# Kernel tuning notes

Hardware: AMD Instinct MI355X
Metric: run time of the kernel (lower is better)

The kernel has to match this reference:

```python
import jax, jax.numpy as jnp
import numpy as np

B, S, D = 32, 1024, 512
LN_EPS = 1e-5


def setup_inputs() -> dict:
    key = jax.random.key(0)
    ks = jax.random.split(key, 12)
    scale = 1.0 / np.sqrt(D)
    return {
        "seq1": jax.random.normal(ks[0], (B, S, D), jnp.float32),
        "seq2": jax.random.normal(ks[1], (B, S, D), jnp.float32),
        "mask1": jax.random.randint(ks[2], (B, S), 0, 2) == 1,
        "mask2": jax.random.randint(ks[3], (B, S), 0, 2) == 1,
        "Wq": jax.random.uniform(ks[4], (D, D), jnp.float32, -scale, scale),
        "bq": jax.random.uniform(ks[5], (D,), jnp.float32, -scale, scale),
        "Wk": jax.random.uniform(ks[6], (D, D), jnp.float32, -scale, scale),
        "bk": jax.random.uniform(ks[7], (D,), jnp.float32, -scale, scale),
        "Wv": jax.random.uniform(ks[8], (D, D), jnp.float32, -scale, scale),
        "bv": jax.random.uniform(ks[9], (D,), jnp.float32, -scale, scale),
        "gamma": jnp.ones((D,), jnp.float32),
        "beta": jnp.zeros((D,), jnp.float32),
    }


def _layernorm(x, gamma, beta):
    mu = jnp.mean(x, axis=-1, keepdims=True)
    var = jnp.mean(jnp.square(x - mu), axis=-1, keepdims=True)
    return (x - mu) * jax.lax.rsqrt(var + LN_EPS) * gamma + beta


def reference(seq1, seq2, mask1, mask2, Wq, bq, Wk, bk, Wv, bv, gamma, beta):
    # relu-projected Q/K/V (shared weights across both sequences)
    q1 = jax.nn.relu(seq1 @ Wq + bq)
    k1 = jax.nn.relu(seq1 @ Wk + bk)
    v1 = jax.nn.relu(seq1 @ Wv + bv)
    q2 = jax.nn.relu(seq2 @ Wq + bq)
    k2 = jax.nn.relu(seq2 @ Wk + bk)
    v2 = jax.nn.relu(seq2 @ Wv + bv)

    # bilinear cross scores: tanh(k1 q2^T) summed over seq2 -> [B,S1]
    a1 = jnp.sum(jnp.tanh(jnp.einsum('bsd,btd->bst', k1, q2)), axis=2)
    a2 = jnp.sum(jnp.tanh(jnp.einsum('btd,bsd->bts', k2, q1)), axis=2)

    a1 = jnp.where(mask1, -jnp.inf, a1)
    a2 = jnp.where(mask2, -jnp.inf, a2)
    a1 = jax.nn.softmax(a1, axis=-1)  # [B,S1]
    a2 = jax.nn.softmax(a2, axis=-1)  # [B,S2]
    # dropout p=0.2 is identity at inference

    vector1 = jnp.einsum('bs,bsd->bd', a1, v1)
    vector2 = jnp.einsum('bs,bsd->bd', a2, v2)

    out1 = _layernorm(jnp.mean(seq1, axis=1) + vector1, gamma, beta)
    out2 = _layernorm(jnp.mean(seq2, axis=1) + vector2, gamma, beta)
    return (out1, out2)
```

## Files before the change

### kernel.cpp

```cpp
#include <hip/hip_runtime.h>


typedef __bf16 bf16x8_t __attribute__((ext_vector_type(8)));
typedef float f32x4_t __attribute__((ext_vector_type(4)));

__device__ __forceinline__ unsigned short f2bf(float f) {
    union { float f; unsigned int u; } c; c.f = f;
    unsigned int u = c.u;
    unsigned int r = (u + 0x7FFFu + ((u >> 16) & 1u)) >> 16;
    return (unsigned short)r;
}
__device__ __forceinline__ float bf2f(unsigned short h) {
    union { unsigned int u; float f; } c; c.u = ((unsigned int)h) << 16;
    return c.f;
}
__device__ __forceinline__ void gl2lds16(const void* g, void* l) {
    __builtin_amdgcn_global_load_lds(
        (const __attribute__((address_space(1))) void*)g,
        (__attribute__((address_space(3))) void*)l, 16, 0, 0);
}
__device__ __forceinline__ float fast_tanh(float x) {
    float e = __expf(2.f * x);
    return 1.f - 2.f * __builtin_amdgcn_rcpf(e + 1.f);
}

__device__ __forceinline__ void stage256(
    const unsigned short* __restrict__ src,
    int k0, unsigned short* dstbase, int wv, int lane)
{
    #pragma unroll
    for (int l = 0; l < 4; ++l) {
        int idx = l * 512 + wv * 64 + lane;
        int row = idx >> 3;
        int kc = (idx & 7) * 8;
        kc ^= ((row >> 2) & 1) << 4;
        gl2lds16(&src[(size_t)row * 512 + k0 + kc],
                 &dstbase[l * 4096 + wv * 512]);
    }
}

template<bool DRAIN>
__device__ __forceinline__ void phase_mfma(
    const unsigned short* A_, const unsigned short* B_,
    f32x4_t acc[8][4], int mh, int nh, int wr, int wc, int qq, int ln)
{
    bf16x8_t af[4][2], bfr[2][2];
    #pragma unroll
    for (int m = 0; m < 4; ++m) {
        int row = wr * 128 + (mh * 4 + m) * 16 + ln;
        #pragma unroll
        for (int ks = 0; ks < 2; ++ks) {
            int e = (row * 64 + ks * 32 + qq * 8) ^ (((row >> 2) & 1) << 4);
            af[m][ks] = *reinterpret_cast<const bf16x8_t*>(&A_[e]);
        }
    }
    #pragma unroll
    for (int n = 0; n < 2; ++n) {
        int row = wc * 64 + (nh * 2 + n) * 16 + ln;
        #pragma unroll
        for (int ks = 0; ks < 2; ++ks) {
            int e = (row * 64 + ks * 32 + qq * 8) ^ (((row >> 2) & 1) << 4);
            bfr[n][ks] = *reinterpret_cast<const bf16x8_t*>(&B_[e]);
        }
    }
    __builtin_amdgcn_s_barrier();
    __builtin_amdgcn_s_setprio(1);
    #pragma unroll
    for (int m = 0; m < 4; ++m)
        #pragma unroll
        for (int n = 0; n < 2; ++n)
            #pragma unroll
            for (int ks = 0; ks < 2; ++ks)
                acc[mh * 4 + m][nh * 2 + n] =
                    __builtin_amdgcn_mfma_f32_16x16x32_bf16(
                        af[m][ks], bfr[n][ks], acc[mh * 4 + m][nh * 2 + n],
                        0, 0, 0);
    __builtin_amdgcn_s_setprio(0);
    if (DRAIN) __syncthreads();
    else       __builtin_amdgcn_s_barrier();
}

#define GEMM256_MAINLOOP(Asrc, Bsrc)                                          \
    stage256(Asrc, 0, &lds[0][0][0], wv, lane);                               \
    stage256(Bsrc, 0, &lds[0][1][0], wv, lane);                               \
    __syncthreads();                                                          \
    _Pragma("unroll")                                                         \
    for (int i = 0; i < 4; ++i) {                                             \
        int kO = (2 * i + 1) * 64;                                            \
        int kE = (2 * i + 2) * 64;                                            \
            \
        stage256(Asrc, kO, &lds[1][0][0], wv, lane);                          \
        phase_mfma<false>(&lds[0][0][0], &lds[0][1][0], acc, 0, 0, wr, wc, qq, ln); \
        stage256(Bsrc, kO, &lds[1][1][0], wv, lane);                          \
        phase_mfma<false>(&lds[0][0][0], &lds[0][1][0], acc, 0, 1, wr, wc, qq, ln); \
        phase_mfma<false>(&lds[0][0][0], &lds[0][1][0], acc, 1, 0, wr, wc, qq, ln); \
        phase_mfma<true >(&lds[0][0][0], &lds[0][1][0], acc, 1, 1, wr, wc, qq, ln); \
            \
        if (i < 3) stage256(Asrc, kE, &lds[0][0][0], wv, lane);               \
        phase_mfma<false>(&lds[1][0][0], &lds[1][1][0], acc, 0, 0, wr, wc, qq, ln); \
        if (i < 3) stage256(Bsrc, kE, &lds[0][1][0], wv, lane);               \
        phase_mfma<false>(&lds[1][0][0], &lds[1][1][0], acc, 0, 1, wr, wc, qq, ln); \
        phase_mfma<false>(&lds[1][0][0], &lds[1][1][0], acc, 1, 0, wr, wc, qq, ln); \
        phase_mfma<true >(&lds[1][0][0], &lds[1][1][0], acc, 1, 1, wr, wc, qq, ln); \
    }

__global__ __launch_bounds__(256) void x2bf_kernel(
    const float* __restrict__ src, unsigned short* __restrict__ dst,
    float* __restrict__ accv)
{
    int chunk = blockIdx.x;
    int b = blockIdx.y;
    int tid = threadIdx.x, lane = tid & 63, wv = tid >> 6;
    __shared__ float red[4][512];
    float sum[8] = {};
    size_t base = ((size_t)b * 1024 + (size_t)chunk * 128) * 512;
    #pragma unroll 4
    for (int i = 0; i < 32; ++i) {
        int r = i * 4 + wv;
        size_t ro = base + (size_t)r * 512;
        float4 a = *reinterpret_cast<const float4*>(&src[ro + lane * 4]);
        float4 c = *reinterpret_cast<const float4*>(&src[ro + 256 + lane * 4]);
        ushort4 ha; ha.x = f2bf(a.x); ha.y = f2bf(a.y); ha.z = f2bf(a.z); ha.w = f2bf(a.w);
        ushort4 hc; hc.x = f2bf(c.x); hc.y = f2bf(c.y); hc.z = f2bf(c.z); hc.w = f2bf(c.w);
        *reinterpret_cast<ushort4*>(&dst[ro + lane * 4]) = ha;
        *reinterpret_cast<ushort4*>(&dst[ro + 256 + lane * 4]) = hc;
        sum[0] += a.x; sum[1] += a.y; sum[2] += a.z; sum[3] += a.w;
        sum[4] += c.x; sum[5] += c.y; sum[6] += c.z; sum[7] += c.w;
    }
    #pragma unroll
    for (int t = 0; t < 4; ++t) {
        red[wv][lane * 4 + t] = sum[t];
        red[wv][256 + lane * 4 + t] = sum[4 + t];
    }
    __syncthreads();
    #pragma unroll
    for (int j = 0; j < 2; ++j) {
        int col = tid + j * 256;
        float s = red[0][col] + red[1][col] + red[2][col] + red[3][col];
        atomicAdd(&accv[(size_t)b * 512 + col], s * (1.f / 1024.f));
    }
}

__global__ __launch_bounds__(256) void wconv_kernel(
    const float* __restrict__ Wq, const float* __restrict__ Wk,
    const float* __restrict__ Wv, unsigned short* __restrict__ Wt)
{
    const float* W = (blockIdx.z == 0) ? Wq : (blockIdx.z == 1) ? Wk : Wv;
    unsigned short* o = Wt + (size_t)blockIdx.z * 512 * 512;
    __shared__ unsigned short t[64][65];
    int k0 = blockIdx.x * 64, n0 = blockIdx.y * 64;
    #pragma unroll
    for (int i = 0; i < 16; ++i) {
        int idx = i * 256 + threadIdx.x;
        int r = idx >> 6, c = idx & 63;
        t[r][c] = f2bf(W[(size_t)(k0 + r) * 512 + n0 + c]);
    }
    __syncthreads();
    #pragma unroll
    for (int i = 0; i < 16; ++i) {
        int idx = i * 256 + threadIdx.x;
        int r = idx >> 6, c = idx & 63;
        o[(size_t)(n0 + r) * 512 + k0 + c] = t[c][r];
    }
}

__global__ __launch_bounds__(512) void biascat_kernel(
    const float* __restrict__ bq, const float* __restrict__ bk,
    const float* __restrict__ bv, float* __restrict__ bc)
{
    int n = threadIdx.x;
    bc[n] = bq[n]; bc[512 + n] = bk[n]; bc[1024 + n] = bv[n];
}

__global__ __launch_bounds__(512, 2) void qkv_gemm(
    const unsigned short* __restrict__ Xb1, const unsigned short* __restrict__ Xb2,
    const unsigned short* __restrict__ Wt, const float* __restrict__ bias_cat,
    unsigned short* __restrict__ qkv)
{
    __shared__ alignas(16) unsigned short lds[2][2][16384];

    unsigned int fid = blockIdx.x;
    unsigned int swz = (fid & 7u) * 192u + (fid >> 3);
    int nt = swz % 6u;
    int mg = swz / 6u;
    int z = mg >> 7;
    int mrow0 = (mg & 127) * 256;
    int n0 = nt * 256;

    const unsigned short* Asrc = (z ? Xb2 : Xb1) + (size_t)mrow0 * 512;
    const unsigned short* Bsrc = Wt + (size_t)n0 * 512;

    int tid = threadIdx.x, lane = tid & 63, wv = tid >> 6;
    int wr = wv >> 2, wc = wv & 3;
    int qq = lane >> 4, ln = lane & 15;

    f32x4_t acc[8][4] = {};

    GEMM256_MAINLOOP(Asrc, Bsrc)

    unsigned short* Ct = &lds[0][0][0];
    #pragma unroll
    for (int ni = 0; ni < 4; ++ni) {
        int col = wc * 64 + ni * 16 + ln;
        float bb = bias_cat[n0 + col];
        #pragma unroll
        for (int mi = 0; mi < 8; ++mi) {
            int row = wr * 128 + mi * 16 + qq * 4;
            #pragma unroll
            for (int r = 0; r < 4; ++r)
                Ct[(row + r) * 256 + col] = f2bf(fmaxf(acc[mi][ni][r] + bb, 0.f));
        }
    }
    __syncthreads();
    int w = nt >> 1, col0 = (nt & 1) * 256;
    unsigned short* outb = qkv + (size_t)(z * 3 + w) * 32768 * 512
                               + (size_t)mrow0 * 512 + col0;
    #pragma unroll
    for (int it = 0; it < 16; ++it) {
        int row = it * 16 + (tid >> 5);
        int ch = tid & 31;
        *reinterpret_cast<uint4*>(&outb[(size_t)row * 512 + ch * 8]) =
            *reinterpret_cast<const uint4*>(&Ct[row * 256 + ch * 8]);
    }
}

__global__ __launch_bounds__(512, 2) void score_kernel(
    const unsigned short* __restrict__ qkv, float* __restrict__ a_out)
{
    __shared__ alignas(16) unsigned short lds[2][2][16384];

    unsigned int fid = blockIdx.x;
    unsigned int swz = (fid & 7u) * 128u + (fid >> 3);
    int tt = swz & 3, st = (swz >> 2) & 3;
    int z = swz >> 4;
    int which = z >> 5, b = z & 31;

    const unsigned short* Asrc =
        qkv + ((size_t)(which ? 4 : 1) * 32768 + (size_t)b * 1024 + st * 256) * 512;
    const unsigned short* Bsrc =
        qkv + ((size_t)(which ? 0 : 3) * 32768 + (size_t)b * 1024 + tt * 256) * 512;

    int tid = threadIdx.x, lane = tid & 63, wv = tid >> 6;
    int wr = wv >> 2, wc = wv & 3;
    int qq = lane >> 4, ln = lane & 15;

    f32x4_t acc[8][4] = {};

    GEMM256_MAINLOOP(Asrc, Bsrc)

    float* arow = a_out + (size_t)z * 1024 + st * 256 + wr * 128;
    #pragma unroll
    for (int mi = 0; mi < 8; ++mi) {
        #pragma unroll
        for (int r = 0; r < 4; ++r) {
            float s = 0.f;
            #pragma unroll
            for (int ni = 0; ni < 4; ++ni) s += fast_tanh(acc[mi][ni][r]);
            #pragma unroll
            for (int off = 1; off <= 8; off <<= 1) s += __shfl_xor(s, off, 64);
            if (ln == 0)
                atomicAdd(&arow[mi * 16 + qq * 4 + r], s);
        }
    }
}

__global__ __launch_bounds__(256) void softmax_kernel(
    const float* __restrict__ a_in, const int* __restrict__ mask1,
    const int* __restrict__ mask2, float* __restrict__ w_out)
{
    int z = blockIdx.x, which = z >> 5, b = z & 31;
    const int* mask = (which ? mask2 : mask1) + (size_t)b * 1024;
    const float* a = a_in + (size_t)z * 1024;
    float* w = w_out + (size_t)z * 1024;
    int tid = threadIdx.x, lane = tid & 63, wv = tid >> 6;

    float vals[4];
    #pragma unroll
    for (int j = 0; j < 4; ++j) {
        int s = tid + j * 256;
        vals[j] = mask[s] ? -__builtin_inff() : a[s];
    }
    float m = fmaxf(fmaxf(vals[0], vals[1]), fmaxf(vals[2], vals[3]));
    #pragma unroll
    for (int off = 32; off; off >>= 1) m = fmaxf(m, __shfl_xor(m, off, 64));
    __shared__ float redm[4], redsum[4];
    if (lane == 0) redm[wv] = m;
    __syncthreads();
    m = fmaxf(fmaxf(redm[0], redm[1]), fmaxf(redm[2], redm[3]));

    float e[4], sum = 0.f;
    #pragma unroll
    for (int j = 0; j < 4; ++j) { e[j] = __expf(vals[j] - m); sum += e[j]; }
    #pragma unroll
    for (int off = 32; off; off >>= 1) sum += __shfl_xor(sum, off, 64);
    if (lane == 0) redsum[wv] = sum;
    __syncthreads();
    sum = redsum[0] + redsum[1] + redsum[2] + redsum[3];
    float inv = 1.f / sum;
    #pragma unroll
    for (int j = 0; j < 4; ++j) w[tid + j * 256] = e[j] * inv;
}

__global__ __launch_bounds__(128) void wsum_kernel(
    const unsigned short* __restrict__ qkv, const float* __restrict__ w_in,
    float* __restrict__ acc)
{
    int chunk = blockIdx.x;
    int z = blockIdx.y, which = z >> 5, b = z & 31;
    const unsigned short* V =
        qkv + ((size_t)(which ? 5 : 2) * 32768 + (size_t)b * 1024) * 512;
    const float* w = w_in + (size_t)z * 1024;
    int d0 = threadIdx.x * 4;
    float a0 = 0.f, a1 = 0.f, a2 = 0.f, a3 = 0.f;
    int s0 = chunk * 128;
    #pragma unroll 4
    for (int s = s0; s < s0 + 128; ++s) {
        ushort4 v = *reinterpret_cast<const ushort4*>(&V[(size_t)s * 512 + d0]);
        float ws = w[s];
        a0 += ws * bf2f(v.x); a1 += ws * bf2f(v.y);
        a2 += ws * bf2f(v.z); a3 += ws * bf2f(v.w);
    }
    atomicAdd(&acc[(size_t)z * 512 + d0 + 0], a0);
    atomicAdd(&acc[(size_t)z * 512 + d0 + 1], a1);
    atomicAdd(&acc[(size_t)z * 512 + d0 + 2], a2);
    atomicAdd(&acc[(size_t)z * 512 + d0 + 3], a3);
}

__global__ __launch_bounds__(512) void ln_kernel(
    const float* __restrict__ acc, const float* __restrict__ gamma,
    const float* __restrict__ beta, float* __restrict__ out)
{
    int z = blockIdx.x, d = threadIdx.x;
    int lane = d & 63, wv = d >> 6;
    float x = acc[(size_t)z * 512 + d];
    float s = x;
    #pragma unroll
    for (int off = 32; off; off >>= 1) s += __shfl_xor(s, off, 64);
    __shared__ float red[8], red2[8];
    if (lane == 0) red[wv] = s;
    __syncthreads();
    float mu = 0.f;
    #pragma unroll
    for (int i = 0; i < 8; ++i) mu += red[i];
    mu *= (1.f / 512.f);
    float c = x - mu;
    float s2 = c * c;
    #pragma unroll
    for (int off = 32; off; off >>= 1) s2 += __shfl_xor(s2, off, 64);
    if (lane == 0) red2[wv] = s2;
    __syncthreads();
    float var = 0.f;
    #pragma unroll
    for (int i = 0; i < 8; ++i) var += red2[i];
    var *= (1.f / 512.f);
    out[(size_t)z * 512 + d] = c * __frsqrt_rn(var + 1e-5f) * gamma[d] + beta[d];
}

extern "C" void kernel_launch(void* const* d_in, const int* in_sizes, int n_in,
                              void* d_out, int out_size, void* d_ws, size_t ws_size,
                              hipStream_t stream) {
    const float* seq1 = (const float*)d_in[0];
    const float* seq2 = (const float*)d_in[1];
    const int* mask1 = (const int*)d_in[2];
    const int* mask2 = (const int*)d_in[3];
    const float* Wq = (const float*)d_in[4];
    const float* bq = (const float*)d_in[5];
    const float* Wk = (const float*)d_in[6];
    const float* bk = (const float*)d_in[7];
    const float* Wv = (const float*)d_in[8];
    const float* bv = (const float*)d_in[9];
    const float* gamma = (const float*)d_in[10];
    const float* beta = (const float*)d_in[11];
    float* out = (float*)d_out;

    char* ws = (char*)d_ws;
    float* a_sc = (float*)(ws);
    float* wsm = (float*)(ws + (256u << 10));
    float* accv = (float*)(ws + (512u << 10));
    float* bias_cat = (float*)(ws + (768u << 10));
    unsigned short* Wt = (unsigned short*)(ws + (1u << 20));
    unsigned short* Xb2 = (unsigned short*)(ws + (4ull << 20));
    unsigned short* qkv = (unsigned short*)(ws + (40ull << 20));
    unsigned short* Xb1 = (unsigned short*)d_in[1];

    hipMemsetAsync(ws, 0, 640u << 10, stream);

    wconv_kernel<<<dim3(8, 8, 3), 256, 0, stream>>>(Wq, Wk, Wv, Wt);
    biascat_kernel<<<1, 512, 0, stream>>>(bq, bk, bv, bias_cat);
    x2bf_kernel<<<dim3(8, 32), 256, 0, stream>>>(seq2, Xb2, accv + 32 * 512);
    x2bf_kernel<<<dim3(8, 32), 256, 0, stream>>>(seq1, Xb1, accv);
    qkv_gemm<<<dim3(1536), 512, 0, stream>>>(Xb1, Xb2, Wt, bias_cat, qkv);
    score_kernel<<<dim3(1024), 512, 0, stream>>>(qkv, a_sc);
    softmax_kernel<<<64, 256, 0, stream>>>(a_sc, mask1, mask2, wsm);
    wsum_kernel<<<dim3(8, 64), 128, 0, stream>>>(qkv, wsm, accv);
    ln_kernel<<<64, 512, 0, stream>>>(accv, gamma, beta, out);
}
```

Baseline: 490.3 us.

## Reuse A/B LDS fragments across MFMA quadrants and widen LDS XOR swizzle

Changes the LDS swizzle from a single-bit XOR on the 16-element chunk to a full 3-bit XOR of the 8-element slot index with the row, to reduce bank conflicts on fragment reads. It also restructures each K-step so A and B fragments are loaded once and reused across quadrants (a0 with b0/b1, a1 with b1/b0), instead of reloading both for every quadrant. The cost is more fragment registers live at once, which may raise register pressure and reduce occupancy.

Result: faster. 436.7 us (-10.9%).

```diff
diff --git a/kernel.cpp b/kernel.cpp
--- a/kernel.cpp
+++ b/kernel.cpp
@@ -32,38 +32,44 @@
     for (int l = 0; l < 4; ++l) {
         int idx = l * 512 + wv * 64 + lane;
         int row = idx >> 3;
-        int kc = (idx & 7) * 8;
-        kc ^= ((row >> 2) & 1) << 4;
-        gl2lds16(&src[(size_t)row * 512 + k0 + kc],
+        int slot = (idx & 7) ^ (row & 7);
+        gl2lds16(&src[(size_t)row * 512 + k0 + slot * 8],
                  &dstbase[l * 4096 + wv * 512]);
     }
 }
 
-template<bool DRAIN>
-__device__ __forceinline__ void phase_mfma(
-    const unsigned short* A_, const unsigned short* B_,
-    f32x4_t acc[8][4], int mh, int nh, int wr, int wc, int qq, int ln)
-{
-    bf16x8_t af[4][2], bfr[2][2];
+__device__ __forceinline__ void read_afrag(
+    const unsigned short* buf, int rbase, int qq, int ln, bf16x8_t af[4][2])
+{
     #pragma unroll
     for (int m = 0; m < 4; ++m) {
-        int row = wr * 128 + (mh * 4 + m) * 16 + ln;
+        int row = rbase + m * 16 + ln;
         #pragma unroll
         for (int ks = 0; ks < 2; ++ks) {
-            int e = (row * 64 + ks * 32 + qq * 8) ^ (((row >> 2) & 1) << 4);
-            af[m][ks] = *reinterpret_cast<const bf16x8_t*>(&A_[e]);
+            int slot = (ks * 4 + qq) ^ (ln & 7);
+            af[m][ks] = *reinterpret_cast<const bf16x8_t*>(
+                &buf[row * 64 + slot * 8]);
         }
     }
+}
+__device__ __forceinline__ void read_bfrag(
+    const unsigned short* buf, int rbase, int qq, int ln, bf16x8_t bfr[2][2])
+{
     #pragma unroll
     for (int n = 0; n < 2; ++n) {
-        int row = wc * 64 + (nh * 2 + n) * 16 + ln;
+        int row = rbase + n * 16 + ln;
         #pragma unroll
         for (int ks = 0; ks < 2; ++ks) {
-            int e = (row * 64 + ks * 32 + qq * 8) ^ (((row >> 2) & 1) << 4);
-            bfr[n][ks] = *reinterpret_cast<const bf16x8_t*>(&B_[e]);
+            int slot = (ks * 4 + qq) ^ (ln & 7);
+            bfr[n][ks] = *reinterpret_cast<const bf16x8_t*>(
+                &buf[row * 64 + slot * 8]);
         }
     }
-    __builtin_amdgcn_s_barrier();
+}
+__device__ __forceinline__ void mfma_quad(
+    const bf16x8_t a[4][2], const bf16x8_t b[2][2],
+    f32x4_t acc[8][4], int mh, int nh)
+{
     __builtin_amdgcn_s_setprio(1);
     #pragma unroll
     for (int m = 0; m < 4; ++m)
@@ -73,12 +79,28 @@
             for (int ks = 0; ks < 2; ++ks)
                 acc[mh * 4 + m][nh * 2 + n] =
                     __builtin_amdgcn_mfma_f32_16x16x32_bf16(
-                        af[m][ks], bfr[n][ks], acc[mh * 4 + m][nh * 2 + n],
-                        0, 0, 0);
+                        a[m][ks], b[n][ks], acc[mh * 4 + m][nh * 2 + n], 0, 0, 0);
     __builtin_amdgcn_s_setprio(0);
-    if (DRAIN) __syncthreads();
-    else       __builtin_amdgcn_s_barrier();
-}
+}
+
+#define GEMM256_HALF(CUR, NXT, SA, SB)                                        \
+    read_afrag(&lds[CUR][0][0], wr * 128, qq, ln, a0);                        \
+    read_bfrag(&lds[CUR][1][0], wc * 64, qq, ln, b0);                         \
+    SA;                                                                       \
+    __builtin_amdgcn_s_barrier();                                             \
+    mfma_quad(a0, b0, acc, 0, 0);                                             \
+    __builtin_amdgcn_s_barrier();                                             \
+    read_bfrag(&lds[CUR][1][0], wc * 64 + 32, qq, ln, b1);                    \
+    SB;                                                                       \
+    __builtin_amdgcn_s_barrier();                                             \
+    mfma_quad(a0, b1, acc, 0, 1);                                             \
+    __builtin_amdgcn_s_barrier();                                             \
+    read_afrag(&lds[CUR][0][0], wr * 128 + 64, qq, ln, a1);                   \
+    __builtin_amdgcn_s_barrier();                                             \
+    mfma_quad(a1, b1, acc, 1, 1);                                             \
+    __builtin_amdgcn_s_barrier();                                             \
+    mfma_quad(a1, b0, acc, 1, 0);                                             \
+    __syncthreads();
 
 #define GEMM256_MAINLOOP(Asrc, Bsrc)                                          \
     stage256(Asrc, 0, &lds[0][0][0], wv, lane);                               \
@@ -88,20 +110,13 @@
     for (int i = 0; i < 4; ++i) {                                             \
         int kO = (2 * i + 1) * 64;                                            \
         int kE = (2 * i + 2) * 64;                                            \
-            \
-        stage256(Asrc, kO, &lds[1][0][0], wv, lane);                          \
-        phase_mfma<false>(&lds[0][0][0], &lds[0][1][0], acc, 0, 0, wr, wc, qq, ln); \
-        stage256(Bsrc, kO, &lds[1][1][0], wv, lane);                          \
-        phase_mfma<false>(&lds[0][0][0], &lds[0][1][0], acc, 0, 1, wr, wc, qq, ln); \
-        phase_mfma<false>(&lds[0][0][0], &lds[0][1][0], acc, 1, 0, wr, wc, qq, ln); \
-        phase_mfma<true >(&lds[0][0][0], &lds[0][1][0], acc, 1, 1, wr, wc, qq, ln); \
-            \
-        if (i < 3) stage256(Asrc, kE, &lds[0][0][0], wv, lane);               \
-        phase_mfma<false>(&lds[1][0][0], &lds[1][1][0], acc, 0, 0, wr, wc, qq, ln); \
-        if (i < 3) stage256(Bsrc, kE, &lds[0][1][0], wv, lane);               \
-        phase_mfma<false>(&lds[1][0][0], &lds[1][1][0], acc, 0, 1, wr, wc, qq, ln); \
-        phase_mfma<false>(&lds[1][0][0], &lds[1][1][0], acc, 1, 0, wr, wc, qq, ln); \
-        phase_mfma<true >(&lds[1][0][0], &lds[1][1][0], acc, 1, 1, wr, wc, qq, ln); \
+        bf16x8_t a0[4][2], a1[4][2], b0[2][2], b1[2][2];                      \
+        GEMM256_HALF(0, 1,                                                    \
+            stage256(Asrc, kO, &lds[1][0][0], wv, lane),                      \
+            stage256(Bsrc, kO, &lds[1][1][0], wv, lane))                      \
+        GEMM256_HALF(1, 0,                                                    \
+            { if (i < 3) stage256(Asrc, kE, &lds[0][0][0], wv, lane); },      \
+            { if (i < 3) stage256(Bsrc, kE, &lds[0][1][0], wv, lane); })      \
     }
 
 __global__ __launch_bounds__(256) void x2bf_kernel(
```

## Replace double-buffered 64-K GEMM mainloop with 4-stage 32-K LDS ring pipeline

Applied to the files above, without the earlier changes.

Both GEMM kernels (QKV projection and cross scores) now share a 4-slot LDS ring. Each stage holds a K-slice of 32 instead of 64, and loads run three stages ahead, gated by explicit vmcnt waits. There is now one barrier per K-step instead of several sub-phase barriers and syncthreads drains, and a new XOR swizzle suits the 32-wide rows. The aim is to hide global-to-LDS latency and cut synchronisation stalls, at the cost of more, smaller MFMA batches and hand-tuned waitcnt counts that must match the number of outstanding loads.

New measurement: 453.1 us. -7.6%, faster.

```diff
diff --git a/kernel.cpp b/kernel.cpp
--- a/kernel.cpp
+++ b/kernel.cpp
@@ -24,85 +24,71 @@
     return 1.f - 2.f * __builtin_amdgcn_rcpf(e + 1.f);
 }
 
-__device__ __forceinline__ void stage256(
+__device__ __forceinline__ void stage32(
     const unsigned short* __restrict__ src,
-    int k0, unsigned short* dstbase, int wv, int lane)
-{
-    #pragma unroll
-    for (int l = 0; l < 4; ++l) {
-        int idx = l * 512 + wv * 64 + lane;
-        int row = idx >> 3;
-        int kc = (idx & 7) * 8;
-        kc ^= ((row >> 2) & 1) << 4;
-        gl2lds16(&src[(size_t)row * 512 + k0 + kc],
+    int k0, unsigned short* dstbase, int tid)
+{
+    int wv = tid >> 6;
+    #pragma unroll
+    for (int l = 0; l < 2; ++l) {
+        int idx = l * 512 + tid;
+        int row = idx >> 2;
+        int slot = (idx & 3) ^ (row & 3);
+        gl2lds16(&src[(size_t)row * 512 + k0 + slot * 8],
                  &dstbase[l * 4096 + wv * 512]);
     }
 }
 
-template<bool DRAIN>
-__device__ __forceinline__ void phase_mfma(
-    const unsigned short* A_, const unsigned short* B_,
-    f32x4_t acc[8][4], int mh, int nh, int wr, int wc, int qq, int ln)
-{
-    bf16x8_t af[4][2], bfr[2][2];
-    #pragma unroll
-    for (int m = 0; m < 4; ++m) {
-        int row = wr * 128 + (mh * 4 + m) * 16 + ln;
-        #pragma unroll
-        for (int ks = 0; ks < 2; ++ks) {
-            int e = (row * 64 + ks * 32 + qq * 8) ^ (((row >> 2) & 1) << 4);
-            af[m][ks] = *reinterpret_cast<const bf16x8_t*>(&A_[e]);
+__device__ __forceinline__ void gemm_ring(
+    const unsigned short* __restrict__ Asrc,
+    const unsigned short* __restrict__ Bsrc,
+    unsigned short (*__restrict__ lds)[2][8192],
+    f32x4_t acc[8][4], int tid, int wr, int wc, int qq, int ln)
+{
+    stage32(Asrc, 0 * 32, &lds[0][0][0], tid);
+    stage32(Bsrc, 0 * 32, &lds[0][1][0], tid);
+    stage32(Asrc, 1 * 32, &lds[1][0][0], tid);
+    stage32(Bsrc, 1 * 32, &lds[1][1][0], tid);
+    stage32(Asrc, 2 * 32, &lds[2][0][0], tid);
+    stage32(Bsrc, 2 * 32, &lds[2][1][0], tid);
+
+    const int slotA = (qq ^ (ln & 3)) * 8;
+
+    #pragma unroll
+    for (int t = 0; t < 16; ++t) {
+        if (t < 14)       asm volatile("s_waitcnt vmcnt(8)" ::: "memory");
+        else if (t == 14) asm volatile("s_waitcnt vmcnt(4)" ::: "memory");
+        else              asm volatile("s_waitcnt vmcnt(0)" ::: "memory");
+        __builtin_amdgcn_s_barrier();
+
+        const unsigned short* A_ = &lds[t & 3][0][0];
+        const unsigned short* B_ = &lds[t & 3][1][0];
+        bf16x8_t af[8], bfr[4];
+        #pragma unroll
+        for (int m = 0; m < 8; ++m)
+            af[m] = *reinterpret_cast<const bf16x8_t*>(
+                &A_[(wr * 128 + m * 16 + ln) * 32 + slotA]);
+        #pragma unroll
+        for (int n = 0; n < 4; ++n)
+            bfr[n] = *reinterpret_cast<const bf16x8_t*>(
+                &B_[(wc * 64 + n * 16 + ln) * 32 + slotA]);
+
+        if (t < 13) {
+            stage32(Asrc, (t + 3) * 32, &lds[(t + 3) & 3][0][0], tid);
+            stage32(Bsrc, (t + 3) * 32, &lds[(t + 3) & 3][1][0], tid);
         }
-    }
-    #pragma unroll
-    for (int n = 0; n < 2; ++n) {
-        int row = wc * 64 + (nh * 2 + n) * 16 + ln;
-        #pragma unroll
-        for (int ks = 0; ks < 2; ++ks) {
-            int e = (row * 64 + ks * 32 + qq * 8) ^ (((row >> 2) & 1) << 4);
-            bfr[n][ks] = *reinterpret_cast<const bf16x8_t*>(&B_[e]);
-        }
-    }
-    __builtin_amdgcn_s_barrier();
-    __builtin_amdgcn_s_setprio(1);
-    #pragma unroll
-    for (int m = 0; m < 4; ++m)
-        #pragma unroll
-        for (int n = 0; n < 2; ++n)
+
+        __builtin_amdgcn_s_setprio(1);
+        #pragma unroll
+        for (int m = 0; m < 8; ++m)
             #pragma unroll
-            for (int ks = 0; ks < 2; ++ks)
-                acc[mh * 4 + m][nh * 2 + n] =
-                    __builtin_amdgcn_mfma_f32_16x16x32_bf16(
-                        af[m][ks], bfr[n][ks], acc[mh * 4 + m][nh * 2 + n],
-                        0, 0, 0);
-    __builtin_amdgcn_s_setprio(0);
-    if (DRAIN) __syncthreads();
-    else       __builtin_amdgcn_s_barrier();
-}
-
-#define GEMM256_MAINLOOP(Asrc, Bsrc)                                          \
-    stage256(Asrc, 0, &lds[0][0][0], wv, lane);                               \
-    stage256(Bsrc, 0, &lds[0][1][0], wv, lane);                               \
-    __syncthreads();                                                          \
-    _Pragma("unroll")                                                         \
-    for (int i = 0; i < 4; ++i) {                                             \
-        int kO = (2 * i + 1) * 64;                                            \
-        int kE = (2 * i + 2) * 64;                                            \
-            \
-        stage256(Asrc, kO, &lds[1][0][0], wv, lane);                          \
-        phase_mfma<false>(&lds[0][0][0], &lds[0][1][0], acc, 0, 0, wr, wc, qq, ln); \
-        stage256(Bsrc, kO, &lds[1][1][0], wv, lane);                          \
-        phase_mfma<false>(&lds[0][0][0], &lds[0][1][0], acc, 0, 1, wr, wc, qq, ln); \
-        phase_mfma<false>(&lds[0][0][0], &lds[0][1][0], acc, 1, 0, wr, wc, qq, ln); \
-        phase_mfma<true >(&lds[0][0][0], &lds[0][1][0], acc, 1, 1, wr, wc, qq, ln); \
-            \
-        if (i < 3) stage256(Asrc, kE, &lds[0][0][0], wv, lane);               \
-        phase_mfma<false>(&lds[1][0][0], &lds[1][1][0], acc, 0, 0, wr, wc, qq, ln); \
-        if (i < 3) stage256(Bsrc, kE, &lds[0][1][0], wv, lane);               \
-        phase_mfma<false>(&lds[1][0][0], &lds[1][1][0], acc, 0, 1, wr, wc, qq, ln); \
-        phase_mfma<false>(&lds[1][0][0], &lds[1][1][0], acc, 1, 0, wr, wc, qq, ln); \
-        phase_mfma<true >(&lds[1][0][0], &lds[1][1][0], acc, 1, 1, wr, wc, qq, ln); \
-    }
+            for (int n = 0; n < 4; ++n)
+                acc[m][n] = __builtin_amdgcn_mfma_f32_16x16x32_bf16(
+                    af[m], bfr[n], acc[m][n], 0, 0, 0);
+        __builtin_amdgcn_s_setprio(0);
+    }
+    __syncthreads();
+}
 
 __global__ __launch_bounds__(256) void x2bf_kernel(
     const float* __restrict__ src, unsigned short* __restrict__ dst,
@@ -177,7 +163,7 @@
     const unsigned short* __restrict__ Wt, const float* __restrict__ bias_cat,
     unsigned short* __restrict__ qkv)
 {
-    __shared__ alignas(16) unsigned short lds[2][2][16384];
+    __shared__ alignas(16) unsigned short lds[4][2][8192];
 
     unsigned int fid = blockIdx.x;
     unsigned int swz = (fid & 7u) * 192u + (fid >> 3);
@@ -193,10 +179,11 @@
     int tid = threadIdx.x, lane = tid & 63, wv = tid >> 6;
     int wr = wv >> 2, wc = wv & 3;
     int qq = lane >> 4, ln = lane & 15;
+    (void)lane;
 
     f32x4_t acc[8][4] = {};
 
-    GEMM256_MAINLOOP(Asrc, Bsrc)
+    gemm_ring(Asrc, Bsrc, lds, acc, tid, wr, wc, qq, ln);
 
     unsigned short* Ct = &lds[0][0][0];
     #pragma unroll
@@ -227,7 +214,7 @@
 __global__ __launch_bounds__(512, 2) void score_kernel(
     const unsigned short* __restrict__ qkv, float* __restrict__ a_out)
 {
-    __shared__ alignas(16) unsigned short lds[2][2][16384];
+    __shared__ alignas(16) unsigned short lds[4][2][8192];
 
     unsigned int fid = blockIdx.x;
     unsigned int swz = (fid & 7u) * 128u + (fid >> 3);
@@ -243,10 +230,11 @@
     int tid = threadIdx.x, lane = tid & 63, wv = tid >> 6;
     int wr = wv >> 2, wc = wv & 3;
     int qq = lane >> 4, ln = lane & 15;
+    (void)lane;
 
     f32x4_t acc[8][4] = {};
 
-    GEMM256_MAINLOOP(Asrc, Bsrc)
+    gemm_ring(Asrc, Bsrc, lds, acc, tid, wr, wc, qq, ln);
 
     float* arow = a_out + (size_t)z * 1024 + st * 256 + wr * 128;
     #pragma unroll
```
